# Kernel tuning notes

Hardware: AMD Instinct MI355X
Metric: run time of the kernel (lower is better)

Reference implementation:

```python
import jax, jax.numpy as jnp
import numpy as np

NUM_LAYERS = 3
CHANNELS = 8
IN_CHANNELS = 8
MASK_OUT_STRIDE = 4


def resize_align_corners(x, oh, ow):
    # Bilinear resize with align_corners=True, x: [N, C, H, W]
    n, c, h, w = x.shape
    ys = jnp.linspace(0.0, h - 1.0, oh)
    xs = jnp.linspace(0.0, w - 1.0, ow)
    y0 = jnp.clip(jnp.floor(ys).astype(jnp.int32), 0, h - 2)
    x0 = jnp.clip(jnp.floor(xs).astype(jnp.int32), 0, w - 2)
    wy = (ys - y0.astype(ys.dtype)).astype(x.dtype)[None, None, :, None]
    wx = (xs - x0.astype(xs.dtype)).astype(x.dtype)[None, None, None, :]
    top = x[:, :, y0, :]
    bot = x[:, :, y0 + 1, :]
    row = top * (1.0 - wy) + bot * wy          # [n,c,oh,w]
    left = row[:, :, :, x0]
    right = row[:, :, :, x0 + 1]
    return left * (1.0 - wx) + right * wx       # [n,c,oh,ow]


def aligned_bilinear(t, factor):
    # Faithful port of adet.utils.comm.aligned_bilinear
    if factor == 1:
        return t
    h, w = t.shape[2], t.shape[3]
    t = jnp.pad(t, ((0, 0), (0, 0), (0, 1), (0, 1)), mode="edge")
    oh, ow = factor * h + 1, factor * w + 1
    t = resize_align_corners(t, oh, ow)
    p = factor // 2
    t = jnp.pad(t, ((0, 0), (0, 0), (p, 0), (p, 0)), mode="edge")
    return t[:, :, : oh - 1, : ow - 1]


def reference(mask_feats, mask_head_params, locations_inst, soi, im_inds, fpn_levels, mask_feat_stride):
    N, C, H, W = mask_feats.shape
    n_inst = mask_head_params.shape[0]
    # compute_locations at mask_feat_stride (x fastest, matching torch meshgrid order)
    half = mask_feat_stride // 2
    sx = jnp.arange(W, dtype=mask_feats.dtype) * mask_feat_stride + half
    sy = jnp.arange(H, dtype=mask_feats.dtype) * mask_feat_stride + half
    gy, gx = jnp.meshgrid(sy, sx, indexing="ij")
    locs = jnp.stack([gx.reshape(-1), gy.reshape(-1)], axis=1)  # [HW, 2]
    # relative coords, normalized by size-of-interest of instance's FPN level
    rel = locations_inst[:, None, :] - locs[None, :, :]          # [n, HW, 2]
    rel = jnp.transpose(rel, (0, 2, 1))                          # [n, 2, HW]
    rel = rel / soi[fpn_levels][:, None, None]
    feats = mask_feats[im_inds].reshape(n_inst, IN_CHANNELS, H * W)
    x = jnp.concatenate([rel.astype(mask_feats.dtype), feats], axis=1)  # [n, 10, HW]
    # parse_dynamic_params: split flat params into per-instance weights/biases
    wn = [(IN_CHANNELS + 2) * CHANNELS, CHANNELS * CHANNELS, CHANNELS * 1]
    bn = [CHANNELS, CHANNELS, 1]
    offs = np.cumsum([0] + wn + bn)
    parts = [mask_head_params[:, offs[i]:offs[i + 1]] for i in range(6)]
    w0 = parts[0].reshape(n_inst, CHANNELS, IN_CHANNELS + 2)
    w1 = parts[1].reshape(n_inst, CHANNELS, CHANNELS)
    w2 = parts[2].reshape(n_inst, 1, CHANNELS)
    b0, b1, b2 = parts[3], parts[4], parts[5]
    # per-instance dynamic MLP (1x1 grouped conv == batched matmul)
    x = jax.nn.relu(jnp.einsum("noi,nip->nop", w0, x) + b0[:, :, None])
    x = jax.nn.relu(jnp.einsum("noi,nip->nop", w1, x) + b1[:, :, None])
    x = jnp.einsum("noi,nip->nop", w2, x) + b2[:, :, None]
    logits = x.reshape(n_inst, 1, H, W)
    factor = int(mask_feat_stride // MASK_OUT_STRIDE)
    return aligned_bilinear(logits, factor)


def setup_inputs() -> dict:
    key = jax.random.key(0)
    k0, k1, k2, k3, k4 = jax.random.split(key, 5)
    N, C, H, W = 4, IN_CHANNELS, 128, 192
    n_inst = 128
    stride = 8
    num_gen_params = (IN_CHANNELS + 2) * CHANNELS + CHANNELS * CHANNELS + CHANNELS + CHANNELS + CHANNELS + 1  # 169
    mask_feats = jax.random.normal(k0, (N, C, H, W), dtype=jnp.float32)
    mask_head_params = jax.random.normal(k1, (n_inst, num_gen_params), dtype=jnp.float32) * 0.1
    locations_inst = jax.random.uniform(k2, (n_inst, 2), dtype=jnp.float32) * jnp.array([W * stride, H * stride], jnp.float32)
    soi = jnp.array([64.0, 128.0, 256.0, 512.0, 1024.0], jnp.float32)
    im_inds = jax.random.randint(k3, (n_inst,), 0, N)
    fpn_levels = jax.random.randint(k4, (n_inst,), 0, 5)
    return {
        "mask_feats": mask_feats,
        "mask_head_params": mask_head_params,
        "locations_inst": locations_inst,
        "soi": soi,
        "im_inds": im_inds,
        "fpn_levels": fpn_levels,
        "mask_feat_stride": stride,
    }
```

## Files before the change

### kernel.cpp

```cpp
#include <hip/hip_runtime.h>

#define HH 128
#define WW 192
#define HW (HH * WW)


__device__ __forceinline__ float relu(float v) { return fmaxf(v, 0.0f); }

__global__ __launch_bounds__(512, 4) void dmh_kernel(
    const float* __restrict__ mask_feats,
    const float* __restrict__ params,
    const float* __restrict__ locs,
    const float* __restrict__ soi,
    const int*   __restrict__ im_inds,
    const int*   __restrict__ fpn_levels,
    const int*   __restrict__ stride_p,
    float*       __restrict__ out)
{
    const int tid = threadIdx.x;
    const int c0 = blockIdx.x * 64;
    const int r0 = blockIdx.y * 32;
    const int n  = blockIdx.z;

    __shared__ float sW[176];
    __shared__ float tile[33 * 66];

    if (tid < 169) {
        float v = params[(size_t)n * 169 + tid];
        int d;
        if (tid < 80)       { int o = tid / 10, r = tid - o * 10;
                              d = (r == 0) ? o : (r == 1) ? (8 + o) : (24 + (r - 2) * 8 + o); }
        else if (tid < 144) { int t = tid - 80, o = t >> 3, i = t & 7; d = 88 + i * 8 + o; }
        else if (tid < 152) d = 152 + (tid - 144);
        else if (tid < 160) d = 16 + (tid - 152);
        else if (tid < 168) d = 160 + (tid - 160);
        else                d = 168;
        sW[d] = v;
    }

    const int   stride = *stride_p;
    const float half   = 0.5f * (float)stride;
    const float locx = locs[2 * n + 0];
    const float locy = locs[2 * n + 1];
    const float inv  = 1.0f / soi[fpn_levels[n]];
    const float* fb  = mask_feats + (size_t)im_inds[n] * 8 * HW;

    __syncthreads();

    {
        const int ir = tid >> 4;
        const int ic = (tid & 15) << 2;
        const int rr = r0 + ir, cc = c0 + ic;
        const float* fp = fb + rr * WW + cc;

        float4 xv[8];
        #pragma unroll
        for (int ch = 0; ch < 8; ++ch)
            xv[ch] = *reinterpret_cast<const float4*>(fp + ch * HW);

        const float rxd = -(float)stride * inv;
        float rx[4];
        rx[0] = (locx - (float)(cc * stride) - half) * inv;
        rx[1] = rx[0] + rxd; rx[2] = rx[1] + rxd; rx[3] = rx[2] + rxd;
        const float ry = (locy - (float)(rr * stride) - half) * inv;

        float h[8][4];
        #pragma unroll
        for (int o = 0; o < 8; ++o) {
            float t  = fmaf(sW[8 + o], ry, sW[16 + o]);
            float wx = sW[o];
            #pragma unroll
            for (int j = 0; j < 4; ++j) h[o][j] = fmaf(wx, rx[j], t);
        }
        #pragma unroll
        for (int ch = 0; ch < 8; ++ch) {
            float4 wlo = *reinterpret_cast<const float4*>(&sW[24 + ch * 8]);
            float4 whi = *reinterpret_cast<const float4*>(&sW[28 + ch * 8]);
            float wv[8] = {wlo.x, wlo.y, wlo.z, wlo.w, whi.x, whi.y, whi.z, whi.w};
            float xj[4] = {xv[ch].x, xv[ch].y, xv[ch].z, xv[ch].w};
            #pragma unroll
            for (int o = 0; o < 8; ++o)
                #pragma unroll
                for (int j = 0; j < 4; ++j) h[o][j] = fmaf(wv[o], xj[j], h[o][j]);
        }

        float a[8][4];
        #pragma unroll
        for (int o = 0; o < 8; ++o) {
            float b = sW[160 + o];
            #pragma unroll
            for (int j = 0; j < 4; ++j) a[o][j] = b;
        }
        #pragma unroll
        for (int i = 0; i < 8; ++i) {
            float4 wlo = *reinterpret_cast<const float4*>(&sW[88 + i * 8]);
            float4 whi = *reinterpret_cast<const float4*>(&sW[92 + i * 8]);
            float wv[8] = {wlo.x, wlo.y, wlo.z, wlo.w, whi.x, whi.y, whi.z, whi.w};
            float vj[4] = {relu(h[i][0]), relu(h[i][1]), relu(h[i][2]), relu(h[i][3])};
            #pragma unroll
            for (int o = 0; o < 8; ++o)
                #pragma unroll
                for (int j = 0; j < 4; ++j) a[o][j] = fmaf(wv[o], vj[j], a[o][j]);
        }

        float b2v = sW[168];
        float lg[4] = {b2v, b2v, b2v, b2v};
        #pragma unroll
        for (int o = 0; o < 8; ++o) {
            float w2 = sW[152 + o];
            #pragma unroll
            for (int j = 0; j < 4; ++j) lg[j] = fmaf(w2, relu(a[o][j]), lg[j]);
        }
        #pragma unroll
        for (int j = 0; j < 4; ++j)
            tile[(ir + 1) * 66 + ic + 1 + j] = lg[j];
    }

    if (tid < 97) {
        int r, c;
        if (tid < 65) { r = -1; c = tid - 1; }
        else          { r = tid - 65; c = -1; }
        int rr = min(max(r0 + r, 0), HH - 1);
        int cc = min(max(c0 + c, 0), WW - 1);
        const float* fp = fb + rr * WW + cc;
        float rx  = (locx - (float)(cc * stride) - half) * inv;
        float ry2 = (locy - (float)(rr * stride) - half) * inv;
        float hh[8];
        #pragma unroll
        for (int o = 0; o < 8; ++o)
            hh[o] = fmaf(sW[o], rx, fmaf(sW[8 + o], ry2, sW[16 + o]));
        #pragma unroll
        for (int ch = 0; ch < 8; ++ch) {
            float x = fp[ch * HW];
            #pragma unroll
            for (int o = 0; o < 8; ++o) hh[o] = fmaf(sW[24 + ch * 8 + o], x, hh[o]);
        }
        float aa[8];
        #pragma unroll
        for (int o = 0; o < 8; ++o) aa[o] = sW[160 + o];
        #pragma unroll
        for (int i = 0; i < 8; ++i) {
            float v = relu(hh[i]);
            #pragma unroll
            for (int o = 0; o < 8; ++o) aa[o] = fmaf(sW[88 + i * 8 + o], v, aa[o]);
        }
        float lg = sW[168];
        #pragma unroll
        for (int o = 0; o < 8; ++o) lg = fmaf(sW[152 + o], relu(aa[o]), lg);
        tile[(r + 1) * 66 + (c + 1)] = lg;
    }
    __syncthreads();

    const int kx = tid & 31;
    const int ky = tid >> 5;
    float* ob = out + ((size_t)n * 256 + 2 * r0) * 384 + 2 * c0 + 4 * kx;
    #pragma unroll
    for (int yy = 0; yy < 4; ++yy) {
        int yt = ky * 4 + yy;
        int i  = 2 * r0 + yt - 1;
        int rb = i >> 1;
        int fy = i & 1;
        float wy0 = fy ? 0.5f : 1.0f;
        float wy1 = fy ? 0.5f : 0.0f;
        int lr  = rb - r0 + 1;
        int lr2 = lr + fy;
        const float* ra = &tile[lr  * 66 + 2 * kx];
        const float* rc = &tile[lr2 * 66 + 2 * kx];
        float t0 = fmaf(wy1, rc[0], wy0 * ra[0]);
        float t1 = fmaf(wy1, rc[1], wy0 * ra[1]);
        float t2 = fmaf(wy1, rc[2], wy0 * ra[2]);
        float4 o4;
        o4.x = 0.5f * (t0 + t1);
        o4.y = t1;
        o4.z = 0.5f * (t1 + t2);
        o4.w = t2;
        *reinterpret_cast<float4*>(ob + (size_t)yt * 384) = o4;
    }
}

extern "C" void kernel_launch(void* const* d_in, const int* in_sizes, int n_in,
                              void* d_out, int out_size, void* d_ws, size_t ws_size,
                              hipStream_t stream) {
    const float* mask_feats = (const float*)d_in[0];
    const float* params     = (const float*)d_in[1];
    const float* locs       = (const float*)d_in[2];
    const float* soi        = (const float*)d_in[3];
    const int*   im_inds    = (const int*)d_in[4];
    const int*   fpn_levels = (const int*)d_in[5];
    const int*   stride_p   = (const int*)d_in[6];
    float* out = (float*)d_out;

    dim3 grid(WW / 64, HH / 32, 128);
    dim3 block(512);
    dmh_kernel<<<grid, block, 0, stream>>>(
        mask_feats, params, locs, soi, im_inds, fpn_levels, stride_p, out);
}
```

Before: 21.10 us.

## Give each wavefront its own weight copy to drop the block barrier

Each 64-lane wavefront now loads and scatters its own copy of the 169 per-instance parameters into a private shared-memory slice. This removes the block-wide __syncthreads between the weight load and the MLP, so each wave relies only on wavefront-level ordering. The feature loads are issued before the weight scatter so their latency overlaps it, and the per-pixel MLP is rewritten with 4-wide vector FMA types. The cost is eight times the weight shared memory and redundant parameter loads, and the code now depends on implicit wave-local ordering of LDS writes and reads with no explicit fence.

```diff
diff --git a/kernel.cpp b/kernel.cpp
--- a/kernel.cpp
+++ b/kernel.cpp
@@ -4,8 +4,17 @@
 #define WW 192
 #define HW (HH * WW)
 
-
+typedef float f32x4 __attribute__((ext_vector_type(4)));
+
+__device__ __forceinline__ f32x4 vfma(f32x4 a, f32x4 b, f32x4 c) {
+    return __builtin_elementwise_fma(a, b, c);
+}
+__device__ __forceinline__ f32x4 splat(float s) { return (f32x4){s, s, s, s}; }
+__device__ __forceinline__ f32x4 vrelu(f32x4 v) {
+    return __builtin_elementwise_max(v, (f32x4){0.f, 0.f, 0.f, 0.f});
+}
 __device__ __forceinline__ float relu(float v) { return fmaxf(v, 0.0f); }
+
 
 __global__ __launch_bounds__(512, 4) void dmh_kernel(
     const float* __restrict__ mask_feats,
@@ -22,20 +31,19 @@
     const int r0 = blockIdx.y * 32;
     const int n  = blockIdx.z;
 
-    __shared__ float sW[176];
+    __shared__ float sW[8 * 176];
     __shared__ float tile[33 * 66];
 
-    if (tid < 169) {
-        float v = params[(size_t)n * 169 + tid];
-        int d;
-        if (tid < 80)       { int o = tid / 10, r = tid - o * 10;
-                              d = (r == 0) ? o : (r == 1) ? (8 + o) : (24 + (r - 2) * 8 + o); }
-        else if (tid < 144) { int t = tid - 80, o = t >> 3, i = t & 7; d = 88 + i * 8 + o; }
-        else if (tid < 152) d = 152 + (tid - 144);
-        else if (tid < 160) d = 16 + (tid - 152);
-        else if (tid < 168) d = 160 + (tid - 160);
-        else                d = 168;
-        sW[d] = v;
+    const int wid  = tid >> 6;
+    const int lane = tid & 63;
+    float* __restrict__ sWb = &sW[wid * 176];
+    const float* __restrict__ P = params + (size_t)n * 169;
+
+    float wval[3];
+    #pragma unroll
+    for (int k = 0; k < 3; ++k) {
+        int idx = lane + 64 * k;
+        wval[k] = (idx < 169) ? P[idx] : 0.0f;
     }
 
     const int   stride = *stride_p;
@@ -45,72 +53,73 @@
     const float inv  = 1.0f / soi[fpn_levels[n]];
     const float* fb  = mask_feats + (size_t)im_inds[n] * 8 * HW;
 
-    __syncthreads();
+    const int ir = tid >> 4;
+    const int ic = (tid & 15) << 2;
+    const int rr = r0 + ir, cc = c0 + ic;
+    const float* fp = fb + rr * WW + cc;
+
+    f32x4 xv[8];
+    #pragma unroll
+    for (int ch = 0; ch < 8; ++ch)
+        xv[ch] = *reinterpret_cast<const f32x4*>(fp + ch * HW);
+
+    #pragma unroll
+    for (int k = 0; k < 3; ++k) {
+        int idx = lane + 64 * k;
+        if (idx < 169) {
+            int d;
+            if (idx < 80)       { int o = idx / 10, r = idx - o * 10;
+                                  d = (r == 0) ? o : (r == 1) ? (8 + o) : (24 + (r - 2) * 8 + o); }
+            else if (idx < 144) { int t = idx - 80, o = t >> 3, i = t & 7; d = 88 + i * 8 + o; }
+            else if (idx < 152) d = 152 + (idx - 144);
+            else if (idx < 160) d = 16 + (idx - 152);
+            else if (idx < 168) d = 160 + (idx - 160);
+            else                d = 168;
+            sWb[d] = wval[k];
+        }
+    }
 
     {
-        const int ir = tid >> 4;
-        const int ic = (tid & 15) << 2;
-        const int rr = r0 + ir, cc = c0 + ic;
-        const float* fp = fb + rr * WW + cc;
-
-        float4 xv[8];
-        #pragma unroll
-        for (int ch = 0; ch < 8; ++ch)
-            xv[ch] = *reinterpret_cast<const float4*>(fp + ch * HW);
-
         const float rxd = -(float)stride * inv;
-        float rx[4];
-        rx[0] = (locx - (float)(cc * stride) - half) * inv;
-        rx[1] = rx[0] + rxd; rx[2] = rx[1] + rxd; rx[3] = rx[2] + rxd;
+        float rx0 = (locx - (float)(cc * stride) - half) * inv;
+        f32x4 rx4 = {rx0, rx0 + rxd, rx0 + 2.f * rxd, rx0 + 3.f * rxd};
         const float ry = (locy - (float)(rr * stride) - half) * inv;
 
-        float h[8][4];
+        f32x4 h[8];
         #pragma unroll
         for (int o = 0; o < 8; ++o) {
-            float t  = fmaf(sW[8 + o], ry, sW[16 + o]);
-            float wx = sW[o];
-            #pragma unroll
-            for (int j = 0; j < 4; ++j) h[o][j] = fmaf(wx, rx[j], t);
+            float t = fmaf(sWb[8 + o], ry, sWb[16 + o]);
+            h[o] = vfma(splat(sWb[o]), rx4, splat(t));
         }
         #pragma unroll
         for (int ch = 0; ch < 8; ++ch) {
-            float4 wlo = *reinterpret_cast<const float4*>(&sW[24 + ch * 8]);
-            float4 whi = *reinterpret_cast<const float4*>(&sW[28 + ch * 8]);
+            float4 wlo = *reinterpret_cast<const float4*>(&sWb[24 + ch * 8]);
+            float4 whi = *reinterpret_cast<const float4*>(&sWb[28 + ch * 8]);
             float wv[8] = {wlo.x, wlo.y, wlo.z, wlo.w, whi.x, whi.y, whi.z, whi.w};
-            float xj[4] = {xv[ch].x, xv[ch].y, xv[ch].z, xv[ch].w};
             #pragma unroll
             for (int o = 0; o < 8; ++o)
-                #pragma unroll
-                for (int j = 0; j < 4; ++j) h[o][j] = fmaf(wv[o], xj[j], h[o][j]);
-        }
-
-        float a[8][4];
-        #pragma unroll
-        for (int o = 0; o < 8; ++o) {
-            float b = sW[160 + o];
-            #pragma unroll
-            for (int j = 0; j < 4; ++j) a[o][j] = b;
-        }
+                h[o] = vfma(splat(wv[o]), xv[ch], h[o]);
+        }
+
+        f32x4 a[8];
+        #pragma unroll
+        for (int o = 0; o < 8; ++o) a[o] = splat(sWb[160 + o]);
         #pragma unroll
         for (int i = 0; i < 8; ++i) {
-            float4 wlo = *reinterpret_cast<const float4*>(&sW[88 + i * 8]);
-            float4 whi = *reinterpret_cast<const float4*>(&sW[92 + i * 8]);
+            float4 wlo = *reinterpret_cast<const float4*>(&sWb[88 + i * 8]);
+            float4 whi = *reinterpret_cast<const float4*>(&sWb[92 + i * 8]);
             float wv[8] = {wlo.x, wlo.y, wlo.z, wlo.w, whi.x, whi.y, whi.z, whi.w};
-            float vj[4] = {relu(h[i][0]), relu(h[i][1]), relu(h[i][2]), relu(h[i][3])};
+            f32x4 v = vrelu(h[i]);
             #pragma unroll
             for (int o = 0; o < 8; ++o)
-                #pragma unroll
-                for (int j = 0; j < 4; ++j) a[o][j] = fmaf(wv[o], vj[j], a[o][j]);
-        }
-
-        float b2v = sW[168];
-        float lg[4] = {b2v, b2v, b2v, b2v};
-        #pragma unroll
-        for (int o = 0; o < 8; ++o) {
-            float w2 = sW[152 + o];
-            #pragma unroll
-            for (int j = 0; j < 4; ++j) lg[j] = fmaf(w2, relu(a[o][j]), lg[j]);
-        }
+                a[o] = vfma(splat(wv[o]), v, a[o]);
+        }
+
+        f32x4 lg = splat(sWb[168]);
+        #pragma unroll
+        for (int o = 0; o < 8; ++o)
+            lg = vfma(splat(sWb[152 + o]), vrelu(a[o]), lg);
+
         #pragma unroll
         for (int j = 0; j < 4; ++j)
             tile[(ir + 1) * 66 + ic + 1 + j] = lg[j];
@@ -120,33 +129,33 @@
         int r, c;
         if (tid < 65) { r = -1; c = tid - 1; }
         else          { r = tid - 65; c = -1; }
-        int rr = min(max(r0 + r, 0), HH - 1);
-        int cc = min(max(c0 + c, 0), WW - 1);
-        const float* fp = fb + rr * WW + cc;
-        float rx  = (locx - (float)(cc * stride) - half) * inv;
-        float ry2 = (locy - (float)(rr * stride) - half) * inv;
+        int hr = min(max(r0 + r, 0), HH - 1);
+        int hc = min(max(c0 + c, 0), WW - 1);
+        const float* hfp = fb + hr * WW + hc;
+        float rx  = (locx - (float)(hc * stride) - half) * inv;
+        float ry2 = (locy - (float)(hr * stride) - half) * inv;
         float hh[8];
         #pragma unroll
         for (int o = 0; o < 8; ++o)
-            hh[o] = fmaf(sW[o], rx, fmaf(sW[8 + o], ry2, sW[16 + o]));
+            hh[o] = fmaf(sWb[o], rx, fmaf(sWb[8 + o], ry2, sWb[16 + o]));
         #pragma unroll
         for (int ch = 0; ch < 8; ++ch) {
-            float x = fp[ch * HW];
-            #pragma unroll
-            for (int o = 0; o < 8; ++o) hh[o] = fmaf(sW[24 + ch * 8 + o], x, hh[o]);
+            float x = hfp[ch * HW];
+            #pragma unroll
+            for (int o = 0; o < 8; ++o) hh[o] = fmaf(sWb[24 + ch * 8 + o], x, hh[o]);
         }
         float aa[8];
         #pragma unroll
-        for (int o = 0; o < 8; ++o) aa[o] = sW[160 + o];
+        for (int o = 0; o < 8; ++o) aa[o] = sWb[160 + o];
         #pragma unroll
         for (int i = 0; i < 8; ++i) {
             float v = relu(hh[i]);
             #pragma unroll
-            for (int o = 0; o < 8; ++o) aa[o] = fmaf(sW[88 + i * 8 + o], v, aa[o]);
-        }
-        float lg = sW[168];
-        #pragma unroll
-        for (int o = 0; o < 8; ++o) lg = fmaf(sW[152 + o], relu(aa[o]), lg);
+            for (int o = 0; o < 8; ++o) aa[o] = fmaf(sWb[88 + i * 8 + o], v, aa[o]);
+        }
+        float lg = sWb[168];
+        #pragma unroll
+        for (int o = 0; o < 8; ++o) lg = fmaf(sWb[152 + o], relu(aa[o]), lg);
         tile[(r + 1) * 66 + (c + 1)] = lg;
     }
     __syncthreads();
```

Measured after the change: 22.49 us. +6.6%, slower.

## Halve block size so each thread computes two rows, and prefetch features before sync

Applied to the files above, without the earlier changes.

The block shrinks from 512 to 256 threads, and each thread now runs the per-pixel MLP for two adjacent rows (8 pixels) instead of one. This reuses shared-memory weight loads and the relative-coordinate setup across more pixels. The global feature loads are issued before the __syncthreads that waits for the weights, so their latency overlaps with the parameter staging. The upsampling loop writes 8 output rows per thread. In exchange, per-thread register use roughly doubles, and there are fewer threads per block to hide latency.

```diff
diff --git a/kernel.cpp b/kernel.cpp
--- a/kernel.cpp
+++ b/kernel.cpp
@@ -4,10 +4,12 @@
 #define WW 192
 #define HW (HH * WW)
 
+typedef float f32x4 __attribute__((ext_vector_type(4)));
 
 __device__ __forceinline__ float relu(float v) { return fmaxf(v, 0.0f); }
 
-__global__ __launch_bounds__(512, 4) void dmh_kernel(
+
+__global__ __launch_bounds__(256, 3) void dmh_kernel(
     const float* __restrict__ mask_feats,
     const float* __restrict__ params,
     const float* __restrict__ locs,
@@ -45,93 +47,128 @@
     const float inv  = 1.0f / soi[fpn_levels[n]];
     const float* fb  = mask_feats + (size_t)im_inds[n] * 8 * HW;
 
+    const int ir  = (tid >> 4) * 2;
+    const int ic  = (tid & 15) * 4;
+    const int rA  = r0 + ir;
+    const int cc0 = c0 + ic;
+    const float* fpA = fb + rA * WW + cc0;
+
+    f32x4 xA[8], xB[8];
+    #pragma unroll
+    for (int ch = 0; ch < 8; ++ch) {
+        xA[ch] = *reinterpret_cast<const f32x4*>(fpA + ch * HW);
+        xB[ch] = *reinterpret_cast<const f32x4*>(fpA + ch * HW + WW);
+    }
+
     __syncthreads();
 
+    const f32x4* __restrict__ sW4 = reinterpret_cast<const f32x4*>(sW);
+
     {
-        const int ir = tid >> 4;
-        const int ic = (tid & 15) << 2;
-        const int rr = r0 + ir, cc = c0 + ic;
-        const float* fp = fb + rr * WW + cc;
-
-        float4 xv[8];
-        #pragma unroll
-        for (int ch = 0; ch < 8; ++ch)
-            xv[ch] = *reinterpret_cast<const float4*>(fp + ch * HW);
-
         const float rxd = -(float)stride * inv;
         float rx[4];
-        rx[0] = (locx - (float)(cc * stride) - half) * inv;
+        rx[0] = (locx - (float)(cc0 * stride) - half) * inv;
         rx[1] = rx[0] + rxd; rx[2] = rx[1] + rxd; rx[3] = rx[2] + rxd;
-        const float ry = (locy - (float)(rr * stride) - half) * inv;
-
-        float h[8][4];
+        const float ryA = (locy - (float)(rA * stride) - half) * inv;
+        const float ryB = ryA - (float)stride * inv;
+
+        f32x4 w0xL = sW4[0], w0xH = sW4[1];
+        f32x4 w0yL = sW4[2], w0yH = sW4[3];
+        f32x4 b0L  = sW4[4], b0H  = sW4[5];
+
+        float hA[8][4], hB[8][4];
         #pragma unroll
         for (int o = 0; o < 8; ++o) {
-            float t  = fmaf(sW[8 + o], ry, sW[16 + o]);
-            float wx = sW[o];
-            #pragma unroll
-            for (int j = 0; j < 4; ++j) h[o][j] = fmaf(wx, rx[j], t);
+            float wx = (o < 4) ? w0xL[o] : w0xH[o - 4];
+            float wy = (o < 4) ? w0yL[o] : w0yH[o - 4];
+            float b  = (o < 4) ? b0L[o]  : b0H[o - 4];
+            float tA = fmaf(wy, ryA, b);
+            float tB = fmaf(wy, ryB, b);
+            #pragma unroll
+            for (int j = 0; j < 4; ++j) {
+                hA[o][j] = fmaf(wx, rx[j], tA);
+                hB[o][j] = fmaf(wx, rx[j], tB);
+            }
         }
         #pragma unroll
         for (int ch = 0; ch < 8; ++ch) {
-            float4 wlo = *reinterpret_cast<const float4*>(&sW[24 + ch * 8]);
-            float4 whi = *reinterpret_cast<const float4*>(&sW[28 + ch * 8]);
-            float wv[8] = {wlo.x, wlo.y, wlo.z, wlo.w, whi.x, whi.y, whi.z, whi.w};
-            float xj[4] = {xv[ch].x, xv[ch].y, xv[ch].z, xv[ch].w};
-            #pragma unroll
-            for (int o = 0; o < 8; ++o)
+            f32x4 wL = sW4[6 + 2 * ch];
+            f32x4 wH = sW4[7 + 2 * ch];
+            #pragma unroll
+            for (int o = 0; o < 8; ++o) {
+                float w = (o < 4) ? wL[o] : wH[o - 4];
                 #pragma unroll
-                for (int j = 0; j < 4; ++j) h[o][j] = fmaf(wv[o], xj[j], h[o][j]);
-        }
-
-        float a[8][4];
+                for (int j = 0; j < 4; ++j) {
+                    hA[o][j] = fmaf(w, xA[ch][j], hA[o][j]);
+                    hB[o][j] = fmaf(w, xB[ch][j], hB[o][j]);
+                }
+            }
+        }
+
+        float aA[8][4], aB[8][4];
+        {
+            f32x4 b1L = sW4[40], b1H = sW4[41];
+            #pragma unroll
+            for (int o = 0; o < 8; ++o) {
+                float b = (o < 4) ? b1L[o] : b1H[o - 4];
+                #pragma unroll
+                for (int j = 0; j < 4; ++j) { aA[o][j] = b; aB[o][j] = b; }
+            }
+        }
+        #pragma unroll
+        for (int i = 0; i < 8; ++i) {
+            f32x4 wL = sW4[22 + 2 * i];
+            f32x4 wH = sW4[23 + 2 * i];
+            float vA[4], vB[4];
+            #pragma unroll
+            for (int j = 0; j < 4; ++j) { vA[j] = relu(hA[i][j]); vB[j] = relu(hB[i][j]); }
+            #pragma unroll
+            for (int o = 0; o < 8; ++o) {
+                float w = (o < 4) ? wL[o] : wH[o - 4];
+                #pragma unroll
+                for (int j = 0; j < 4; ++j) {
+                    aA[o][j] = fmaf(w, vA[j], aA[o][j]);
+                    aB[o][j] = fmaf(w, vB[j], aB[o][j]);
+                }
+            }
+        }
+
+        f32x4 w2L = sW4[38], w2H = sW4[39];
+        const float b2v = sW[168];
+        float lgA[4] = {b2v, b2v, b2v, b2v};
+        float lgB[4] = {b2v, b2v, b2v, b2v};
         #pragma unroll
         for (int o = 0; o < 8; ++o) {
-            float b = sW[160 + o];
-            #pragma unroll
-            for (int j = 0; j < 4; ++j) a[o][j] = b;
-        }
-        #pragma unroll
-        for (int i = 0; i < 8; ++i) {
-            float4 wlo = *reinterpret_cast<const float4*>(&sW[88 + i * 8]);
-            float4 whi = *reinterpret_cast<const float4*>(&sW[92 + i * 8]);
-            float wv[8] = {wlo.x, wlo.y, wlo.z, wlo.w, whi.x, whi.y, whi.z, whi.w};
-            float vj[4] = {relu(h[i][0]), relu(h[i][1]), relu(h[i][2]), relu(h[i][3])};
-            #pragma unroll
-            for (int o = 0; o < 8; ++o)
-                #pragma unroll
-                for (int j = 0; j < 4; ++j) a[o][j] = fmaf(wv[o], vj[j], a[o][j]);
-        }
-
-        float b2v = sW[168];
-        float lg[4] = {b2v, b2v, b2v, b2v};
-        #pragma unroll
-        for (int o = 0; o < 8; ++o) {
-            float w2 = sW[152 + o];
-            #pragma unroll
-            for (int j = 0; j < 4; ++j) lg[j] = fmaf(w2, relu(a[o][j]), lg[j]);
-        }
-        #pragma unroll
-        for (int j = 0; j < 4; ++j)
-            tile[(ir + 1) * 66 + ic + 1 + j] = lg[j];
+            float w2 = (o < 4) ? w2L[o] : w2H[o - 4];
+            #pragma unroll
+            for (int j = 0; j < 4; ++j) {
+                lgA[j] = fmaf(w2, relu(aA[o][j]), lgA[j]);
+                lgB[j] = fmaf(w2, relu(aB[o][j]), lgB[j]);
+            }
+        }
+        #pragma unroll
+        for (int j = 0; j < 4; ++j) {
+            tile[(ir + 1) * 66 + ic + 1 + j] = lgA[j];
+            tile[(ir + 2) * 66 + ic + 1 + j] = lgB[j];
+        }
     }
 
     if (tid < 97) {
         int r, c;
         if (tid < 65) { r = -1; c = tid - 1; }
         else          { r = tid - 65; c = -1; }
-        int rr = min(max(r0 + r, 0), HH - 1);
-        int cc = min(max(c0 + c, 0), WW - 1);
-        const float* fp = fb + rr * WW + cc;
-        float rx  = (locx - (float)(cc * stride) - half) * inv;
-        float ry2 = (locy - (float)(rr * stride) - half) * inv;
+        int hr = min(max(r0 + r, 0), HH - 1);
+        int hc = min(max(c0 + c, 0), WW - 1);
+        const float* hfp = fb + hr * WW + hc;
+        float rx  = (locx - (float)(hc * stride) - half) * inv;
+        float ry2 = (locy - (float)(hr * stride) - half) * inv;
         float hh[8];
         #pragma unroll
         for (int o = 0; o < 8; ++o)
             hh[o] = fmaf(sW[o], rx, fmaf(sW[8 + o], ry2, sW[16 + o]));
         #pragma unroll
         for (int ch = 0; ch < 8; ++ch) {
-            float x = fp[ch * HW];
+            float x = hfp[ch * HW];
             #pragma unroll
             for (int o = 0; o < 8; ++o) hh[o] = fmaf(sW[24 + ch * 8 + o], x, hh[o]);
         }
@@ -155,17 +192,17 @@
     const int ky = tid >> 5;
     float* ob = out + ((size_t)n * 256 + 2 * r0) * 384 + 2 * c0 + 4 * kx;
     #pragma unroll
-    for (int yy = 0; yy < 4; ++yy) {
-        int yt = ky * 4 + yy;
-        int i  = 2 * r0 + yt - 1;
-        int rb = i >> 1;
-        int fy = i & 1;
+    for (int yy = 0; yy < 8; ++yy) {
+        int yt = ky * 8 + yy;
+        int iy = yt - 1;
+        int rbl = iy >> 1;
+        int fy = iy & 1;
         float wy0 = fy ? 0.5f : 1.0f;
         float wy1 = fy ? 0.5f : 0.0f;
-        int lr  = rb - r0 + 1;
-        int lr2 = lr + fy;
-        const float* ra = &tile[lr  * 66 + 2 * kx];
-        const float* rc = &tile[lr2 * 66 + 2 * kx];
+        int sr  = rbl + 1;
+        int sr2 = sr + fy;
+        const float* ra = &tile[sr  * 66 + 2 * kx];
+        const float* rc = &tile[sr2 * 66 + 2 * kx];
         float t0 = fmaf(wy1, rc[0], wy0 * ra[0]);
         float t1 = fmaf(wy1, rc[1], wy0 * ra[1]);
         float t2 = fmaf(wy1, rc[2], wy0 * ra[2]);
@@ -191,7 +228,7 @@
     float* out = (float*)d_out;
 
     dim3 grid(WW / 64, HH / 32, 128);
-    dim3 block(512);
+    dim3 block(256);
     dmh_kernel<<<grid, block, 0, stream>>>(
         mask_feats, params, locs, soi, im_inds, fpn_levels, stride_p, out);
 }
```

Result: slower. 24.92 us (+18.1%).

## Shrink tiles to 16x32 with 2 pixels per thread and hoist feature loads

Applied to the files above, without the earlier changes.

Halves the block to 256 threads covering a 16x32 tile, with each thread computing 2 pixels instead of 4. It also moves the global feature and parameter loads ahead of the shared-memory weight scatter and barrier so their latency overlaps that setup. The intent is to raise occupancy and cut register pressure, at the cost of relatively more halo recomputation (49 halo pixels per 512 interior instead of 97 per 2048) and more blocks overall.

```diff
diff --git a/kernel.cpp b/kernel.cpp
--- a/kernel.cpp
+++ b/kernel.cpp
@@ -4,10 +4,12 @@
 #define WW 192
 #define HW (HH * WW)
 
+typedef float f32x2 __attribute__((ext_vector_type(2)));
 
 __device__ __forceinline__ float relu(float v) { return fmaxf(v, 0.0f); }
 
-__global__ __launch_bounds__(512, 4) void dmh_kernel(
+
+__global__ __launch_bounds__(256, 8) void dmh_kernel(
     const float* __restrict__ mask_feats,
     const float* __restrict__ params,
     const float* __restrict__ locs,
@@ -18,15 +20,35 @@
     float*       __restrict__ out)
 {
     const int tid = threadIdx.x;
-    const int c0 = blockIdx.x * 64;
-    const int r0 = blockIdx.y * 32;
+    const int c0 = blockIdx.x * 32;
+    const int r0 = blockIdx.y * 16;
     const int n  = blockIdx.z;
 
     __shared__ float sW[176];
-    __shared__ float tile[33 * 66];
+    __shared__ float tile[17 * 34];
+
+    float wv = 0.0f;
+    if (tid < 169) wv = params[(size_t)n * 169 + tid];
+
+    const int   stride = *stride_p;
+    const float half   = 0.5f * (float)stride;
+    const float locx = locs[2 * n + 0];
+    const float locy = locs[2 * n + 1];
+    const float inv  = 1.0f / soi[fpn_levels[n]];
+    const float* fb  = mask_feats + (size_t)im_inds[n] * 8 * HW;
+
+    const int row = tid >> 4;
+    const int cp  = tid & 15;
+    const int rr  = r0 + row;
+    const int cc  = c0 + 2 * cp;
+    const float* fp = fb + rr * WW + cc;
+
+    f32x2 xv[8];
+    #pragma unroll
+    for (int ch = 0; ch < 8; ++ch)
+        xv[ch] = *reinterpret_cast<const f32x2*>(fp + ch * HW);
 
     if (tid < 169) {
-        float v = params[(size_t)n * 169 + tid];
         int d;
         if (tid < 80)       { int o = tid / 10, r = tid - o * 10;
                               d = (r == 0) ? o : (r == 1) ? (8 + o) : (24 + (r - 2) * 8 + o); }
@@ -35,103 +57,77 @@
         else if (tid < 160) d = 16 + (tid - 152);
         else if (tid < 168) d = 160 + (tid - 160);
         else                d = 168;
-        sW[d] = v;
+        sW[d] = wv;
     }
-
-    const int   stride = *stride_p;
-    const float half   = 0.5f * (float)stride;
-    const float locx = locs[2 * n + 0];
-    const float locy = locs[2 * n + 1];
-    const float inv  = 1.0f / soi[fpn_levels[n]];
-    const float* fb  = mask_feats + (size_t)im_inds[n] * 8 * HW;
-
     __syncthreads();
 
     {
-        const int ir = tid >> 4;
-        const int ic = (tid & 15) << 2;
-        const int rr = r0 + ir, cc = c0 + ic;
-        const float* fp = fb + rr * WW + cc;
-
-        float4 xv[8];
-        #pragma unroll
-        for (int ch = 0; ch < 8; ++ch)
-            xv[ch] = *reinterpret_cast<const float4*>(fp + ch * HW);
-
         const float rxd = -(float)stride * inv;
-        float rx[4];
-        rx[0] = (locx - (float)(cc * stride) - half) * inv;
-        rx[1] = rx[0] + rxd; rx[2] = rx[1] + rxd; rx[3] = rx[2] + rxd;
+        float rx0 = (locx - (float)(cc * stride) - half) * inv;
+        float rx1 = rx0 + rxd;
         const float ry = (locy - (float)(rr * stride) - half) * inv;
 
-        float h[8][4];
+        float h[8][2];
         #pragma unroll
         for (int o = 0; o < 8; ++o) {
-            float t  = fmaf(sW[8 + o], ry, sW[16 + o]);
-            float wx = sW[o];
-            #pragma unroll
-            for (int j = 0; j < 4; ++j) h[o][j] = fmaf(wx, rx[j], t);
+            float t = fmaf(sW[8 + o], ry, sW[16 + o]);
+            h[o][0] = fmaf(sW[o], rx0, t);
+            h[o][1] = fmaf(sW[o], rx1, t);
         }
         #pragma unroll
         for (int ch = 0; ch < 8; ++ch) {
-            float4 wlo = *reinterpret_cast<const float4*>(&sW[24 + ch * 8]);
-            float4 whi = *reinterpret_cast<const float4*>(&sW[28 + ch * 8]);
-            float wv[8] = {wlo.x, wlo.y, wlo.z, wlo.w, whi.x, whi.y, whi.z, whi.w};
-            float xj[4] = {xv[ch].x, xv[ch].y, xv[ch].z, xv[ch].w};
+            float x0 = xv[ch][0], x1 = xv[ch][1];
             #pragma unroll
-            for (int o = 0; o < 8; ++o)
-                #pragma unroll
-                for (int j = 0; j < 4; ++j) h[o][j] = fmaf(wv[o], xj[j], h[o][j]);
+            for (int o = 0; o < 8; ++o) {
+                float w = sW[24 + ch * 8 + o];
+                h[o][0] = fmaf(w, x0, h[o][0]);
+                h[o][1] = fmaf(w, x1, h[o][1]);
+            }
         }
-
-        float a[8][4];
+        float a[8][2];
         #pragma unroll
         for (int o = 0; o < 8; ++o) {
             float b = sW[160 + o];
-            #pragma unroll
-            for (int j = 0; j < 4; ++j) a[o][j] = b;
+            a[o][0] = b; a[o][1] = b;
         }
         #pragma unroll
         for (int i = 0; i < 8; ++i) {
-            float4 wlo = *reinterpret_cast<const float4*>(&sW[88 + i * 8]);
-            float4 whi = *reinterpret_cast<const float4*>(&sW[92 + i * 8]);
-            float wv[8] = {wlo.x, wlo.y, wlo.z, wlo.w, whi.x, whi.y, whi.z, whi.w};
-            float vj[4] = {relu(h[i][0]), relu(h[i][1]), relu(h[i][2]), relu(h[i][3])};
+            float v0 = relu(h[i][0]);
+            float v1 = relu(h[i][1]);
             #pragma unroll
-            for (int o = 0; o < 8; ++o)
-                #pragma unroll
-                for (int j = 0; j < 4; ++j) a[o][j] = fmaf(wv[o], vj[j], a[o][j]);
+            for (int o = 0; o < 8; ++o) {
+                float w = sW[88 + i * 8 + o];
+                a[o][0] = fmaf(w, v0, a[o][0]);
+                a[o][1] = fmaf(w, v1, a[o][1]);
+            }
         }
-
-        float b2v = sW[168];
-        float lg[4] = {b2v, b2v, b2v, b2v};
+        float lg0 = sW[168], lg1 = lg0;
         #pragma unroll
         for (int o = 0; o < 8; ++o) {
             float w2 = sW[152 + o];
-            #pragma unroll
-            for (int j = 0; j < 4; ++j) lg[j] = fmaf(w2, relu(a[o][j]), lg[j]);
+            lg0 = fmaf(w2, relu(a[o][0]), lg0);
+            lg1 = fmaf(w2, relu(a[o][1]), lg1);
         }
-        #pragma unroll
-        for (int j = 0; j < 4; ++j)
-            tile[(ir + 1) * 66 + ic + 1 + j] = lg[j];
+        tile[(row + 1) * 34 + 2 * cp + 1] = lg0;
+        tile[(row + 1) * 34 + 2 * cp + 2] = lg1;
     }
 
-    if (tid < 97) {
+    if (tid < 49) {
         int r, c;
-        if (tid < 65) { r = -1; c = tid - 1; }
-        else          { r = tid - 65; c = -1; }
-        int rr = min(max(r0 + r, 0), HH - 1);
-        int cc = min(max(c0 + c, 0), WW - 1);
-        const float* fp = fb + rr * WW + cc;
-        float rx  = (locx - (float)(cc * stride) - half) * inv;
-        float ry2 = (locy - (float)(rr * stride) - half) * inv;
+        if (tid < 33) { r = -1; c = tid - 1; }
+        else          { r = tid - 33; c = -1; }
+        int hr = min(max(r0 + r, 0), HH - 1);
+        int hc = min(max(c0 + c, 0), WW - 1);
+        const float* hfp = fb + hr * WW + hc;
+        float rx  = (locx - (float)(hc * stride) - half) * inv;
+        float ry2 = (locy - (float)(hr * stride) - half) * inv;
         float hh[8];
         #pragma unroll
         for (int o = 0; o < 8; ++o)
             hh[o] = fmaf(sW[o], rx, fmaf(sW[8 + o], ry2, sW[16 + o]));
         #pragma unroll
         for (int ch = 0; ch < 8; ++ch) {
-            float x = fp[ch * HW];
+            float x = hfp[ch * HW];
             #pragma unroll
             for (int o = 0; o < 8; ++o) hh[o] = fmaf(sW[24 + ch * 8 + o], x, hh[o]);
         }
@@ -147,25 +143,25 @@
         float lg = sW[168];
         #pragma unroll
         for (int o = 0; o < 8; ++o) lg = fmaf(sW[152 + o], relu(aa[o]), lg);
-        tile[(r + 1) * 66 + (c + 1)] = lg;
+        tile[(r + 1) * 34 + (c + 1)] = lg;
     }
     __syncthreads();
 
-    const int kx = tid & 31;
-    const int ky = tid >> 5;
+    const int kx = tid & 15;
+    const int ky = tid >> 4;
     float* ob = out + ((size_t)n * 256 + 2 * r0) * 384 + 2 * c0 + 4 * kx;
     #pragma unroll
-    for (int yy = 0; yy < 4; ++yy) {
-        int yt = ky * 4 + yy;
-        int i  = 2 * r0 + yt - 1;
-        int rb = i >> 1;
-        int fy = i & 1;
+    for (int yy = 0; yy < 2; ++yy) {
+        int yt = ky * 2 + yy;
+        int iy = 2 * r0 + yt - 1;
+        int rbl = iy >> 1;
+        int fy = iy & 1;
         float wy0 = fy ? 0.5f : 1.0f;
         float wy1 = fy ? 0.5f : 0.0f;
-        int lr  = rb - r0 + 1;
-        int lr2 = lr + fy;
-        const float* ra = &tile[lr  * 66 + 2 * kx];
-        const float* rc = &tile[lr2 * 66 + 2 * kx];
+        int sr  = rbl - r0 + 1;
+        int sr2 = sr + fy;
+        const float* ra = &tile[sr  * 34 + 2 * kx];
+        const float* rc = &tile[sr2 * 34 + 2 * kx];
         float t0 = fmaf(wy1, rc[0], wy0 * ra[0]);
         float t1 = fmaf(wy1, rc[1], wy0 * ra[1]);
         float t2 = fmaf(wy1, rc[2], wy0 * ra[2]);
@@ -190,8 +186,8 @@
     const int*   stride_p   = (const int*)d_in[6];
     float* out = (float*)d_out;
 
-    dim3 grid(WW / 64, HH / 32, 128);
-    dim3 block(512);
+    dim3 grid(WW / 32, HH / 16, 128);
+    dim3 block(256);
     dmh_kernel<<<grid, block, 0, stream>>>(
         mask_feats, params, locs, soi, im_inds, fpn_levels, stride_p, out);
 }
```

Result: slower. 24.12 us (+14.3%).
